# Performance work log

Measured on AMD Instinct MI355X. Metric: run time of the kernel, lower is better.

The kernel has to match this reference:

```python
import jax, jax.numpy as jnp
import numpy as np

NEG_MASK = -9e15
ALPHA = 0.2  # LeakyReLU negative slope


def _gat_layer(h, adj, W, a):
    # h: [B,K,Fin], adj: [B,K,K], W: [Fin,F], a: [2F]
    Wh = jnp.einsum('bki,io->bko', h, W)            # [B,K,F]
    F = Wh.shape[-1]
    a_src, a_dst = a[:F], a[F:]
    # e_ij = LeakyReLU(a . [Wh_i || Wh_j]) = LeakyReLU(Wh_i.a_src + Wh_j.a_dst)
    f_src = Wh @ a_src                              # [B,K]
    f_dst = Wh @ a_dst                              # [B,K]
    e = jax.nn.leaky_relu(f_src[:, :, None] + f_dst[:, None, :], ALPHA)  # [B,K,K]
    e = jnp.where(adj > 0, e, NEG_MASK)
    att = jax.nn.softmax(e, axis=2)                 # softmax over neighbors j
    # dropout is identity in eval mode (training=False)
    h_prime = jnp.einsum('bkj,bjo->bko', att, Wh)   # [B,K,F]
    return jax.nn.elu(h_prime)


def setup_inputs() -> dict:
    key = jax.random.key(0)
    ks = jax.random.split(key, 6)
    B, K, Fin, H, Fout = 128, 512, 224, 64, 32
    x = jax.random.normal(ks[0], (B, K, Fin), dtype=jnp.float32)
    adj = jax.random.randint(ks[1], (B, K, K), 0, 2, dtype=jnp.int32)
    W1 = jax.random.normal(ks[2], (Fin, H), dtype=jnp.float32) * (1.0 / np.sqrt(Fin))
    a1 = jax.random.normal(ks[3], (2 * H,), dtype=jnp.float32) * 0.1
    W2 = jax.random.normal(ks[4], (H, Fout), dtype=jnp.float32) * (1.0 / np.sqrt(H))
    a2 = jax.random.normal(ks[5], (2 * Fout,), dtype=jnp.float32) * 0.1
    return {"x": x, "adj": adj, "W1": W1, "a1": a1, "W2": W2, "a2": a2}


def reference(x, adj, W1, a1, W2, a2):
    h = _gat_layer(x, adj, W1, a1)   # conv1: in -> hidden
    h = _gat_layer(h, adj, W2, a2)   # conv2: hidden -> out
    return h
```

## Files before the change

kernel.cpp:

```cpp
#include <hip/hip_runtime.h>
#include <stdint.h>


#define B_   128
#define K_   512
#define FIN  224
#define H1   64
#define H2   32

typedef float    f32x4 __attribute__((ext_vector_type(4)));
typedef short    s16x8 __attribute__((ext_vector_type(8)));
typedef unsigned short u16;

__device__ __forceinline__ u16 f2bf(float f){
  uint32_t u = __float_as_uint(f);
  u += 0x7FFFu + ((u >> 16) & 1u);
  return (u16)(u >> 16);
}
__device__ __forceinline__ float bf2f(u16 h){ return __uint_as_float(((uint32_t)h) << 16); }

__global__ __launch_bounds__(256) void k_bitmask(const int* __restrict__ adj, uint32_t* __restrict__ bits){
  const int t = threadIdx.x, l = t & 63, w = t >> 6;
  const int4* ap = reinterpret_cast<const int4*>(adj) + (size_t)blockIdx.x * 4096 + t;
#pragma unroll 4
  for (int it = 0; it < 16; ++it){
    int4 v = ap[it * 256];
    uint32_t nib = (v.x != 0 ? 1u : 0u) | (v.y != 0 ? 2u : 0u) | (v.z != 0 ? 4u : 0u) | (v.w != 0 ? 8u : 0u);
    uint32_t val = nib << ((l & 7) * 4);
    val |= __shfl_xor(val, 1);
    val |= __shfl_xor(val, 2);
    val |= __shfl_xor(val, 4);
    if ((l & 7) == 0)
      bits[(size_t)blockIdx.x * 512 + it * 32 + w * 8 + (l >> 3)] = val;
  }
}

__global__ __launch_bounds__(256) void k_prep(const float* __restrict__ W1, const float* __restrict__ W2,
                                              u16* __restrict__ W1T, u16* __restrict__ W2T){
  int t = blockIdx.x * 256 + threadIdx.x;
  if (t < FIN * H1){ int k = t / H1, o = t % H1; W1T[o * FIN + k] = f2bf(W1[t]); }
  else { int u = t - FIN * H1; if (u < H1 * H2){ int k = u / H2, o = u % H2; W2T[o * H1 + k] = f2bf(W2[u]); } }
}

template<int KD, int NO, bool AF32>
__global__ __launch_bounds__(256) void k_gemm(const void* __restrict__ Ain, const u16* __restrict__ WT,
                                              const float* __restrict__ avec,
                                              u16* __restrict__ WhT, float* __restrict__ fs, float* __restrict__ fd){
  const int tid = threadIdx.x;
  const int wid = tid >> 6, lane = tid & 63;
  const int g = lane >> 4, lr = lane & 15;
  const size_t row0 = (size_t)blockIdx.x * 64;
  const size_t arow = row0 + 16 * wid + lr;

  f32x4 acc[NO / 16];
#pragma unroll
  for (int c = 0; c < NO/16; ++c) acc[c] = (f32x4){0.f, 0.f, 0.f, 0.f};

#pragma unroll
  for (int s = 0; s < KD / 32; ++s){
    const int k0 = s * 32 + 8 * g;
    s16x8 af;
    if (AF32){
      const float* A = (const float*)Ain;
      float4 v0 = *(const float4*)(A + arow * KD + k0);
      float4 v1 = *(const float4*)(A + arow * KD + k0 + 4);
      af[0] = (short)f2bf(v0.x); af[1] = (short)f2bf(v0.y); af[2] = (short)f2bf(v0.z); af[3] = (short)f2bf(v0.w);
      af[4] = (short)f2bf(v1.x); af[5] = (short)f2bf(v1.y); af[6] = (short)f2bf(v1.z); af[7] = (short)f2bf(v1.w);
    } else {
      af = *(const s16x8*)((const u16*)Ain + arow * KD + k0);
    }
#pragma unroll
    for (int c = 0; c < NO/16; ++c){
      const s16x8 bf = *(const s16x8*)(WT + (size_t)(16 * c + lr) * KD + k0);
      acc[c] = __builtin_amdgcn_mfma_f32_16x16x32_bf16(af, bf, acc[c], 0, 0, 0);
    }
  }

  const size_t b = row0 >> 9;
  const int krow0 = (int)(row0 & 511) + 16 * wid + 4 * g;
  float fsp[4] = {0.f,0.f,0.f,0.f}, fdp[4] = {0.f,0.f,0.f,0.f};
#pragma unroll
  for (int c = 0; c < NO/16; ++c){
    const int o = 16 * c + lr;
    const float as = avec[o], ad = avec[NO + o];
#pragma unroll
    for (int r = 0; r < 4; ++r){
      fsp[r] += acc[c][r] * as;
      fdp[r] += acc[c][r] * ad;
      WhT[(b * NO + o) * K_ + krow0 + r] = f2bf(acc[c][r]);
    }
  }
#pragma unroll
  for (int m = 1; m < 16; m <<= 1){
#pragma unroll
    for (int r = 0; r < 4; ++r){ fsp[r] += __shfl_xor(fsp[r], m); fdp[r] += __shfl_xor(fdp[r], m); }
  }
  if (lr == 0){
#pragma unroll
    for (int r = 0; r < 4; ++r){
      size_t row = row0 + 16 * wid + 4 * g + r;
      fs[row] = fsp[r]; fd[row] = fdp[r];
    }
  }
}

template<int NO, bool OUTBF>
__global__ __launch_bounds__(256) void k_attn(const u16* __restrict__ WhT, const float* __restrict__ fsv,
                                              const float* __restrict__ fdv, const uint32_t* __restrict__ bits,
                                              void* __restrict__ outp){
  const int tid = threadIdx.x;
  const int wid = tid >> 6, lane = tid & 63;
  const int g = lane >> 4, lr = lane & 15;
  const int b = blockIdx.x >> 3;
  const int i0 = (blockIdx.x & 7) * 64;
  const int irow = i0 + 16 * wid + lr;
  const float fsr = fsv[(size_t)b * K_ + irow];
  const uint32_t* brow = bits + ((size_t)b * K_ + irow) * 16;
  const float* fdb = fdv + (size_t)b * K_;
  const u16* whb = WhT + (size_t)b * NO * K_;

  f32x4 acc[NO / 16];
#pragma unroll
  for (int c = 0; c < NO/16; ++c) acc[c] = (f32x4){0.f, 0.f, 0.f, 0.f};
  float lsum = 0.f;

  for (int st = 0; st < 16; ++st){
    const int j0 = st * 32 + 8 * g;
    const uint32_t byte = (brow[st] >> (8 * g)) & 0xFFu;
    float4 fd0 = *(const float4*)(fdb + j0);
    float4 fd1 = *(const float4*)(fdb + j0 + 4);
    float pv[8] = { fd0.x, fd0.y, fd0.z, fd0.w, fd1.x, fd1.y, fd1.z, fd1.w };
    s16x8 bp;
    float lacc = 0.f;
#pragma unroll
    for (int e = 0; e < 8; ++e){
      float sc = fsr + pv[e];
      sc = fmaxf(sc, 0.2f * sc);
      float pe = __expf(sc - 8.0f);
      pe = ((byte >> e) & 1u) ? pe : 0.f;
      u16 h = f2bf(pe);
      bp[e] = (short)h;
      lacc += bf2f(h);
    }
    lsum += lacc;
#pragma unroll
    for (int c = 0; c < NO/16; ++c){
      const s16x8 aw = *(const s16x8*)(whb + (size_t)(16 * c + lr) * K_ + j0);
      acc[c] = __builtin_amdgcn_mfma_f32_16x16x32_bf16(aw, bp, acc[c], 0, 0, 0);
    }
  }

  lsum += __shfl_xor(lsum, 16);
  lsum += __shfl_xor(lsum, 32);
  const float inv = 1.0f / lsum;

#pragma unroll
  for (int c = 0; c < NO/16; ++c){
#pragma unroll
    for (int r = 0; r < 4; ++r){
      float v = acc[c][r] * inv;
      v = v > 0.f ? v : (__expf(v) - 1.0f);
      const size_t idx = ((size_t)b * K_ + irow) * NO + 16 * c + 4 * g + r;
      if (OUTBF) ((u16*)outp)[idx] = f2bf(v);
      else       ((float*)outp)[idx] = v;
    }
  }
}

extern "C" void kernel_launch(void* const* d_in, const int* in_sizes, int n_in,
                              void* d_out, int out_size, void* d_ws, size_t ws_size,
                              hipStream_t stream){
  const float* x   = (const float*)d_in[0];
  const int*   adj = (const int*)  d_in[1];
  const float* W1  = (const float*)d_in[2];
  const float* a1  = (const float*)d_in[3];
  const float* W2  = (const float*)d_in[4];
  const float* a2  = (const float*)d_in[5];
  float* out = (float*)d_out;

  char* ws = (char*)d_ws;
  u16*      WhT1 = (u16*)     (ws);
  u16*      h1   = (u16*)     (ws + 8388608);
  u16*      WhT2 = (u16*)     (ws + 16777216);
  uint32_t* bits = (uint32_t*)(ws + 20971520);
  float*    fs1  = (float*)   (ws + 25165824);
  float*    fd1  = (float*)   (ws + 25427968);
  float*    fs2  = (float*)   (ws + 25690112);
  float*    fd2  = (float*)   (ws + 25952256);
  u16*      W1T  = (u16*)     (ws + 26214400);
  u16*      W2T  = (u16*)     (ws + 26243072);

  k_bitmask<<<dim3(2048), dim3(256), 0, stream>>>(adj, bits);
  k_prep   <<<dim3(64),   dim3(256), 0, stream>>>(W1, W2, W1T, W2T);
  k_gemm<FIN, H1, true >  <<<dim3(1024), dim3(256), 0, stream>>>((const void*)x,  W1T, a1, WhT1, fs1, fd1);
  k_attn<H1, true >       <<<dim3(1024), dim3(256), 0, stream>>>(WhT1, fs1, fd1, bits, (void*)h1);
  k_gemm<H1,  H2, false>  <<<dim3(1024), dim3(256), 0, stream>>>((const void*)h1, W2T, a2, WhT2, fs2, fd2);
  k_attn<H2, false>       <<<dim3(1024), dim3(256), 0, stream>>>(WhT2, fs2, fd2, bits, (void*)out);
}
```

Measured before the change: 325.2 us.

## Store weights, Wh and adjacency bits in MFMA-fragment-ordered layouts

Weights and the intermediate Wh tensors are stored in a fragment-major layout, so each MFMA operand load becomes one contiguous 16-byte-per-lane read instead of a strided row gather. The adjacency bitmask is transposed so that lanes reading consecutive rows hit consecutive words. Output and Wh stores are packed into vector writes. The cost is more complex index math in the producer kernels, and the Wh writes are now scattered 8-byte chunks.

```diff
diff --git a/kernel.cpp b/kernel.cpp
--- a/kernel.cpp
+++ b/kernel.cpp
@@ -19,33 +19,40 @@
 }
 __device__ __forceinline__ float bf2f(u16 h){ return __uint_as_float(((uint32_t)h) << 16); }
 
-__global__ __launch_bounds__(256) void k_bitmask(const int* __restrict__ adj, uint32_t* __restrict__ bits){
-  const int t = threadIdx.x, l = t & 63, w = t >> 6;
-  const int4* ap = reinterpret_cast<const int4*>(adj) + (size_t)blockIdx.x * 4096 + t;
+__device__ __forceinline__ int fragoff(int o, int k, int NO){
+  return (((k >> 5) * (NO >> 4) + (o >> 4)) << 9) + (((o & 15) + (((k & 31) >> 3) << 4)) << 3) + (k & 7);
+}
+
+__global__ __launch_bounds__(256) void k_bitmask(const int* __restrict__ adj, uint32_t* __restrict__ bits2){
+  const int t = threadIdx.x;
 #pragma unroll 4
   for (int it = 0; it < 16; ++it){
-    int4 v = ap[it * 256];
+    const size_t q = (size_t)blockIdx.x * 4096 + it * 256 + t;
+    int4 v = reinterpret_cast<const int4*>(adj)[q];
     uint32_t nib = (v.x != 0 ? 1u : 0u) | (v.y != 0 ? 2u : 0u) | (v.z != 0 ? 4u : 0u) | (v.w != 0 ? 8u : 0u);
-    uint32_t val = nib << ((l & 7) * 4);
+    uint32_t val = nib << ((t & 7) * 4);
     val |= __shfl_xor(val, 1);
     val |= __shfl_xor(val, 2);
     val |= __shfl_xor(val, 4);
-    if ((l & 7) == 0)
-      bits[(size_t)blockIdx.x * 512 + it * 32 + w * 8 + (l >> 3)] = val;
+    if ((t & 7) == 0){
+      const size_t qw = q >> 3;
+      const int st = (int)(qw & 15), i = (int)((qw >> 4) & 511), b = (int)(qw >> 13);
+      bits2[((size_t)(b * 16 + st) << 9) + i] = val;
+    }
   }
 }
 
 __global__ __launch_bounds__(256) void k_prep(const float* __restrict__ W1, const float* __restrict__ W2,
-                                              u16* __restrict__ W1T, u16* __restrict__ W2T){
+                                              u16* __restrict__ W1F, u16* __restrict__ W2F){
   int t = blockIdx.x * 256 + threadIdx.x;
-  if (t < FIN * H1){ int k = t / H1, o = t % H1; W1T[o * FIN + k] = f2bf(W1[t]); }
-  else { int u = t - FIN * H1; if (u < H1 * H2){ int k = u / H2, o = u % H2; W2T[o * H1 + k] = f2bf(W2[u]); } }
+  if (t < FIN * H1){ int k = t / H1, o = t % H1; W1F[fragoff(o, k, H1)] = f2bf(W1[t]); }
+  else { int u = t - FIN * H1; if (u < H1 * H2){ int k = u / H2, o = u % H2; W2F[fragoff(o, k, H2)] = f2bf(W2[u]); } }
 }
 
 template<int KD, int NO, bool AF32>
-__global__ __launch_bounds__(256) void k_gemm(const void* __restrict__ Ain, const u16* __restrict__ WT,
+__global__ __launch_bounds__(256) void k_gemm(const void* __restrict__ Ain, const u16* __restrict__ WF,
                                               const float* __restrict__ avec,
-                                              u16* __restrict__ WhT, float* __restrict__ fs, float* __restrict__ fd){
+                                              u16* __restrict__ WhF, float* __restrict__ fs, float* __restrict__ fd){
   const int tid = threadIdx.x;
   const int wid = tid >> 6, lane = tid & 63;
   const int g = lane >> 4, lr = lane & 15;
@@ -71,7 +78,7 @@
     }
 #pragma unroll
     for (int c = 0; c < NO/16; ++c){
-      const s16x8 bf = *(const s16x8*)(WT + (size_t)(16 * c + lr) * KD + k0);
+      const s16x8 bf = *(const s16x8*)(WF + ((s * (NO/16) + c) << 9) + lane * 8);
       acc[c] = __builtin_amdgcn_mfma_f32_16x16x32_bf16(af, bf, acc[c], 0, 0, 0);
     }
   }
@@ -84,11 +91,11 @@
     const int o = 16 * c + lr;
     const float as = avec[o], ad = avec[NO + o];
 #pragma unroll
-    for (int r = 0; r < 4; ++r){
-      fsp[r] += acc[c][r] * as;
-      fdp[r] += acc[c][r] * ad;
-      WhT[(b * NO + o) * K_ + krow0 + r] = f2bf(acc[c][r]);
-    }
+    for (int r = 0; r < 4; ++r){ fsp[r] += acc[c][r] * as; fdp[r] += acc[c][r] * ad; }
+    uint2 pk;
+    pk.x = (uint32_t)f2bf(acc[c][0]) | ((uint32_t)f2bf(acc[c][1]) << 16);
+    pk.y = (uint32_t)f2bf(acc[c][2]) | ((uint32_t)f2bf(acc[c][3]) << 16);
+    *(uint2*)(WhF + b * (NO * 512) + fragoff(o, krow0, NO)) = pk;
   }
 #pragma unroll
   for (int m = 1; m < 16; m <<= 1){
@@ -105,8 +112,8 @@
 }
 
 template<int NO, bool OUTBF>
-__global__ __launch_bounds__(256) void k_attn(const u16* __restrict__ WhT, const float* __restrict__ fsv,
-                                              const float* __restrict__ fdv, const uint32_t* __restrict__ bits,
+__global__ __launch_bounds__(256) void k_attn(const u16* __restrict__ WhF, const float* __restrict__ fsv,
+                                              const float* __restrict__ fdv, const uint32_t* __restrict__ bits2,
                                               void* __restrict__ outp){
   const int tid = threadIdx.x;
   const int wid = tid >> 6, lane = tid & 63;
@@ -115,9 +122,9 @@
   const int i0 = (blockIdx.x & 7) * 64;
   const int irow = i0 + 16 * wid + lr;
   const float fsr = fsv[(size_t)b * K_ + irow];
-  const uint32_t* brow = bits + ((size_t)b * K_ + irow) * 16;
   const float* fdb = fdv + (size_t)b * K_;
-  const u16* whb = WhT + (size_t)b * NO * K_;
+  const uint32_t* bb = bits2 + ((size_t)b * 16 << 9);
+  const u16* whb = WhF + (size_t)b * (NO * 512);
 
   f32x4 acc[NO / 16];
 #pragma unroll
@@ -126,7 +133,7 @@
 
   for (int st = 0; st < 16; ++st){
     const int j0 = st * 32 + 8 * g;
-    const uint32_t byte = (brow[st] >> (8 * g)) & 0xFFu;
+    const uint32_t byte = (bb[(st << 9) + irow] >> (8 * g)) & 0xFFu;
     float4 fd0 = *(const float4*)(fdb + j0);
     float4 fd1 = *(const float4*)(fdb + j0 + 4);
     float pv[8] = { fd0.x, fd0.y, fd0.z, fd0.w, fd1.x, fd1.y, fd1.z, fd1.w };
@@ -145,7 +152,7 @@
     lsum += lacc;
 #pragma unroll
     for (int c = 0; c < NO/16; ++c){
-      const s16x8 aw = *(const s16x8*)(whb + (size_t)(16 * c + lr) * K_ + j0);
+      const s16x8 aw = *(const s16x8*)(whb + ((st * (NO/16) + c) << 9) + lane * 8);
       acc[c] = __builtin_amdgcn_mfma_f32_16x16x32_bf16(aw, bp, acc[c], 0, 0, 0);
     }
   }
@@ -156,13 +163,20 @@
 
 #pragma unroll
   for (int c = 0; c < NO/16; ++c){
+    float v[4];
 #pragma unroll
     for (int r = 0; r < 4; ++r){
-      float v = acc[c][r] * inv;
-      v = v > 0.f ? v : (__expf(v) - 1.0f);
-      const size_t idx = ((size_t)b * K_ + irow) * NO + 16 * c + 4 * g + r;
-      if (OUTBF) ((u16*)outp)[idx] = f2bf(v);
-      else       ((float*)outp)[idx] = v;
+      float t = acc[c][r] * inv;
+      v[r] = t > 0.f ? t : (__expf(t) - 1.0f);
+    }
+    const size_t base = ((size_t)b * K_ + irow) * NO + 16 * c + 4 * g;
+    if (OUTBF){
+      uint2 pk;
+      pk.x = (uint32_t)f2bf(v[0]) | ((uint32_t)f2bf(v[1]) << 16);
+      pk.y = (uint32_t)f2bf(v[2]) | ((uint32_t)f2bf(v[3]) << 16);
+      *(uint2*)((u16*)outp + base) = pk;
+    } else {
+      *(float4*)((float*)outp + base) = (float4){v[0], v[1], v[2], v[3]};
     }
   }
 }
@@ -179,21 +193,21 @@
   float* out = (float*)d_out;
 
   char* ws = (char*)d_ws;
-  u16*      WhT1 = (u16*)     (ws);
+  u16*      WhF1 = (u16*)     (ws);
   u16*      h1   = (u16*)     (ws + 8388608);
-  u16*      WhT2 = (u16*)     (ws + 16777216);
+  u16*      WhF2 = (u16*)     (ws + 16777216);
   uint32_t* bits = (uint32_t*)(ws + 20971520);
   float*    fs1  = (float*)   (ws + 25165824);
   float*    fd1  = (float*)   (ws + 25427968);
   float*    fs2  = (float*)   (ws + 25690112);
   float*    fd2  = (float*)   (ws + 25952256);
-  u16*      W1T  = (u16*)     (ws + 26214400);
-  u16*      W2T  = (u16*)     (ws + 26243072);
+  u16*      W1F  = (u16*)     (ws + 26214400);
+  u16*      W2F  = (u16*)     (ws + 26243072);
 
   k_bitmask<<<dim3(2048), dim3(256), 0, stream>>>(adj, bits);
-  k_prep   <<<dim3(64),   dim3(256), 0, stream>>>(W1, W2, W1T, W2T);
-  k_gemm<FIN, H1, true >  <<<dim3(1024), dim3(256), 0, stream>>>((const void*)x,  W1T, a1, WhT1, fs1, fd1);
-  k_attn<H1, true >       <<<dim3(1024), dim3(256), 0, stream>>>(WhT1, fs1, fd1, bits, (void*)h1);
-  k_gemm<H1,  H2, false>  <<<dim3(1024), dim3(256), 0, stream>>>((const void*)h1, W2T, a2, WhT2, fs2, fd2);
-  k_attn<H2, false>       <<<dim3(1024), dim3(256), 0, stream>>>(WhT2, fs2, fd2, bits, (void*)out);
-}
+  k_prep   <<<dim3(64),   dim3(256), 0, stream>>>(W1, W2, W1F, W2F);
+  k_gemm<FIN, H1, true >  <<<dim3(1024), dim3(256), 0, stream>>>((const void*)x,  W1F, a1, WhF1, fs1, fd1);
+  k_attn<H1, true >       <<<dim3(1024), dim3(256), 0, stream>>>(WhF1, fs1, fd1, bits, (void*)h1);
+  k_gemm<H1,  H2, false>  <<<dim3(1024), dim3(256), 0, stream>>>((const void*)h1, W2F, a2, WhF2, fs2, fd2);
+  k_attn<H2, false>       <<<dim3(1024), dim3(256), 0, stream>>>(WhF2, fs2, fd2, bits, (void*)out);
+}
```

Result: faster. 293.9 us (-9.6%).
